# Optimization experiments

Measured on AMD Instinct MI355X. Metric: run time of the kernel, lower is better.

## Reference

```python
import jax, jax.numpy as jnp
import numpy as np
import math

V, L, D, S, F, H, B = 32000, 6, 1024, 2048, 4096, 16, 2
DK = D // H
EPS = 1e-5


def _pos_encoding(max_len, d_model):
    pos = np.arange(max_len)[:, None].astype(np.float32)
    freq = np.exp(np.arange(0, d_model, 2).astype(np.float32) * -(math.log(10000.0) / d_model))
    pe = np.zeros((max_len, d_model), dtype=np.float32)
    pe[:, 0::2] = np.sin(pos * freq)
    pe[:, 1::2] = np.cos(pos * freq)
    return jnp.asarray(pe)


def setup_inputs() -> dict:
    key = jax.random.key(0)
    ks = jax.random.split(key, 16)
    n = lambda k, shape: (jax.random.normal(k, shape, dtype=jnp.float32) * 0.02)
    return {
        "tokens": jax.random.randint(ks[0], (B, S), 0, V, dtype=jnp.int32),
        "emb": n(ks[1], (V, D)),
        "Wq": n(ks[2], (L, D, D)), "bq": jnp.zeros((L, D)),
        "Wk": n(ks[3], (L, D, D)), "bk": jnp.zeros((L, D)),
        "Wv": n(ks[4], (L, D, D)), "bv": jnp.zeros((L, D)),
        "Wo": n(ks[5], (L, D, D)), "bo": jnp.zeros((L, D)),
        "W1": n(ks[6], (L, D, F)), "b1": jnp.zeros((L, F)),
        "W2": n(ks[7], (L, F, D)), "b2": jnp.zeros((L, D)),
        "g1": jnp.ones((L, D)), "be1": jnp.zeros((L, D)),
        "g2": jnp.ones((L, D)), "be2": jnp.zeros((L, D)),
    }


def _layernorm(x, g, b):
    mu = jnp.mean(x, axis=-1, keepdims=True)
    var = jnp.var(x, axis=-1, keepdims=True)
    return (x - mu) * jax.lax.rsqrt(var + EPS) * g + b


def _encoder(tokens, emb, Wq, bq, Wk, bk, Wv, bv, Wo, bo, W1, b1, W2, b2, g1, be1, g2, be2):
    pe = _pos_encoding(S, D)
    x = emb[tokens] * jnp.float32(math.sqrt(D)) + pe  # [B,S,D]

    def layer(x, p):
        wq, bq_, wk, bk_, wv, bv_, wo, bo_, w1, b1_, w2, b2_, g1_, be1_, g2_, be2_ = p
        q = (x @ wq + bq_).reshape(B, S, H, DK)
        k = (x @ wk + bk_).reshape(B, S, H, DK)
        v = (x @ wv + bv_).reshape(B, S, H, DK)
        scores = jnp.einsum("bqhd,bkhd->bhqk", q, k) / jnp.float32(math.sqrt(DK))
        attn = jax.nn.softmax(scores, axis=-1)
        out = jnp.einsum("bhqk,bkhd->bqhd", attn, v).reshape(B, S, D)
        out = out @ wo + bo_
        x = _layernorm(x + out, g1_, be1_)
        ff = jax.nn.relu(x @ w1 + b1_) @ w2 + b2_
        x = _layernorm(x + ff, g2_, be2_)
        return x, None

    params = (Wq, bq, Wk, bk, Wv, bv, Wo, bo, W1, b1, W2, b2, g1, be1, g2, be2)
    x, _ = jax.lax.scan(layer, x, params)
    return x


def reference(tokens, emb, Wq, bq, Wk, bk, Wv, bv, Wo, bo, W1, b1, W2, b2, g1, be1, g2, be2):
    return _encoder(tokens, emb, Wq, bq, Wk, bk, Wv, bv, Wo, bo, W1, b1, W2, b2, g1, be1, g2, be2)
```

## Files before the change

kernel.cpp:

```cpp
#include <hip/hip_runtime.h>
#include <hip/hip_bf16.h>

#define DEV static __device__ __forceinline__

typedef __attribute__((ext_vector_type(8))) short bf16x8;
typedef __attribute__((ext_vector_type(4))) float f32x4;
typedef __attribute__((ext_vector_type(4))) unsigned short u16x4;
typedef __attribute__((ext_vector_type(4))) unsigned int u32x4;

constexpr int Lc = 6, Dc = 1024, Sc = 2048, Fc = 4096, Hc = 16, Bc = 2;
constexpr int Mc = Bc * Sc;
constexpr int QKVN = 3 * Dc;
constexpr float QSCALE = 0.18033688011112042f;

DEV float bf2f(unsigned short u) {
  unsigned int x = ((unsigned int)u) << 16; float f;
  __builtin_memcpy(&f, &x, 4); return f;
}
DEV unsigned short f2bf(float f) {
  unsigned int x; __builtin_memcpy(&x, &f, 4);
  x += 0x7fffu + ((x >> 16) & 1u);
  return (unsigned short)(x >> 16);
}
DEV unsigned int cvt_pk_bf16(float lo, float hi) {
  unsigned int r;
  asm("v_cvt_pk_bf16_f32 %0, %1, %2" : "=v"(r) : "v"(lo), "v"(hi));
  return r;
}

typedef __attribute__((address_space(1))) unsigned int* gas_t;
typedef __attribute__((address_space(3))) unsigned int* las_t;
DEV void gload16(const void* g, void* l) {
  __builtin_amdgcn_global_load_lds((gas_t)g, (las_t)l, 16, 0, 0);
}

__global__ __launch_bounds__(256) void transpose_f2b(
    const float* __restrict__ W, unsigned short* __restrict__ Wt,
    int Kd, int Nd, float scale)
{
  __shared__ float tile[32][33];
  const int n0 = blockIdx.x * 32, k0 = blockIdx.y * 32;
  const int tx = threadIdx.x & 31, ty = threadIdx.x >> 5;
#pragma unroll
  for (int i = 0; i < 4; ++i) {
    int k = ty + i * 8;
    tile[k][tx] = W[(size_t)(k0 + k) * Nd + n0 + tx];
  }
  __syncthreads();
#pragma unroll
  for (int i = 0; i < 4; ++i) {
    int n = ty + i * 8;
    Wt[(size_t)(n0 + n) * Kd + k0 + tx] = f2bf(tile[tx][n] * scale);
  }
}

DEV int vperm(int k) {
  return ((k >> 5) << 5) + (((k >> 2) & 3) << 3) + (((k >> 4) & 1) << 2) + (k & 3);
}
__global__ __launch_bounds__(256) void transpose_v(
    const unsigned short* __restrict__ QKV, unsigned short* __restrict__ Vt)
{
  __shared__ unsigned short tile[32][33];
  const int s0 = blockIdx.x * 32, c0 = blockIdx.y * 32, b = blockIdx.z;
  const int tx = threadIdx.x & 31, ty = threadIdx.x >> 5;
  const unsigned short* src = QKV + ((size_t)b * Sc) * QKVN + 2 * Dc;
#pragma unroll
  for (int i = 0; i < 4; ++i) {
    int s = ty + i * 8;
    tile[s][tx] = src[(size_t)(s0 + s) * QKVN + c0 + tx];
  }
  __syncthreads();
  unsigned short* dst = Vt + (size_t)b * Dc * Sc;
  const int s = s0 + tx;
  const int sp = (s & ~63) + vperm(s & 63);
#pragma unroll
  for (int i = 0; i < 4; ++i) {
    int c = ty + i * 8;
    dst[(size_t)(c0 + c) * Sc + sp] = tile[tx][c];
  }
}

__global__ __launch_bounds__(256) void pack_bias(
    const float* __restrict__ bq, const float* __restrict__ bk,
    const float* __restrict__ bv, float* __restrict__ out)
{
  int i = blockIdx.x * 256 + threadIdx.x;
  out[i] = (i < Dc) ? bq[i] * QSCALE : (i < 2 * Dc ? bk[i - Dc] : bv[i - 2 * Dc]);
}

__global__ __launch_bounds__(256) void embed_kernel(
    const int* __restrict__ tokens, const float* __restrict__ emb,
    float* __restrict__ xf, unsigned short* __restrict__ xb)
{
  const int bs = blockIdx.x;
  const int s = bs & (Sc - 1);
  const int tok = tokens[bs];
  const int d0 = threadIdx.x * 4;
  f32x4 e4 = *(const f32x4*)(emb + (size_t)tok * Dc + d0);
  f32x4 vf; u16x4 vb;
#pragma unroll
  for (int j = 0; j < 4; ++j) {
    int d = d0 + j;
    float e = e4[j] * 32.0f;
    float fr = expf((float)(d & ~1) * (-9.210340371976184f / 1024.0f));
    float arg = (float)s * fr;
    float pe = (d & 1) ? cosf(arg) : sinf(arg);
    float v = e + pe;
    vf[j] = v; vb[j] = f2bf(v);
  }
  *(f32x4*)(xf + (size_t)bs * Dc + d0) = vf;
  *(u16x4*)(xb + (size_t)bs * Dc + d0) = vb;
}

DEV void gemm_core(const unsigned short* A, const unsigned short* Bt,
                   unsigned short* As, unsigned short* Bs,
                   f32x4 (*acc)[4], int mTile, int nTile,
                   int Kstride, int k0, int k1, int t)
{
  const int lane = t & 63;
  const int w = t >> 6;
  const int wm = w >> 1, wn = w & 1;
  for (int kt = k0; kt < k1; kt += 64) {
    __syncthreads();
#pragma unroll
    for (int i = 0; i < 4; ++i) {
      int idx = i * 256 + t;
      int row = idx >> 3;
      int sl = (idx & 7) ^ (row & 7);
      gload16(A + (size_t)(mTile + row) * Kstride + kt + sl * 8, &As[idx * 8]);
      gload16(Bt + (size_t)(nTile + row) * Kstride + kt + sl * 8, &Bs[idx * 8]);
    }
    __syncthreads();
#pragma unroll
    for (int ks = 0; ks < 2; ++ks) {
      const int kb = ks * 64 + ((lane >> 4) << 4);
      bf16x8 a[4], b[4];
#pragma unroll
      for (int mi = 0; mi < 4; ++mi) {
        int r = wm * 64 + mi * 16 + (lane & 15);
        a[mi] = *(const bf16x8*)((const char*)As + r * 128 + (kb ^ ((r & 7) << 4)));
      }
#pragma unroll
      for (int ni = 0; ni < 4; ++ni) {
        int r = wn * 64 + ni * 16 + (lane & 15);
        b[ni] = *(const bf16x8*)((const char*)Bs + r * 128 + (kb ^ ((r & 7) << 4)));
      }
#pragma unroll
      for (int mi = 0; mi < 4; ++mi)
#pragma unroll
        for (int ni = 0; ni < 4; ++ni)
          acc[mi][ni] = __builtin_amdgcn_mfma_f32_16x16x32_bf16(
              a[mi], b[ni], acc[mi][ni], 0, 0, 0);
    }
  }
}

__global__ __launch_bounds__(256) void gemm128(
    const unsigned short* __restrict__ A, const unsigned short* __restrict__ Bt,
    const float* __restrict__ bias, unsigned short* __restrict__ outB,
    int gx, int Ndim, int Kdim, int relu)
{
  __shared__ alignas(16) unsigned short As[128 * 64];
  __shared__ alignas(16) unsigned short Bs[128 * 64];
  const int t = threadIdx.x;
  const int lane = t & 63;
  const int w = t >> 6;
  const int wm = w >> 1, wn = w & 1;
  const int nwg = gridDim.x, flat = blockIdx.x;
  const int swz = (flat & 7) * (nwg >> 3) + (flat >> 3);
  const int mTile = (swz / gx) * 128;
  const int nTile = (swz % gx) * 128;

  f32x4 acc[4][4] = {};
  gemm_core(A, Bt, As, Bs, acc, mTile, nTile, Kdim, 0, Kdim, t);

#pragma unroll
  for (int mi = 0; mi < 4; ++mi) {
#pragma unroll
    for (int ni = 0; ni < 4; ++ni) {
      const int c = nTile + wn * 64 + ni * 16 + (lane & 15);
      const float bvv = bias[c];
#pragma unroll
      for (int j = 0; j < 4; ++j) {
        const int r = mTile + wm * 64 + mi * 16 + ((lane >> 4) << 2) + j;
        float v = acc[mi][ni][j] + bvv;
        if (relu) v = fmaxf(v, 0.0f);
        outB[(size_t)r * Ndim + c] = f2bf(v);
      }
    }
  }
}

template<int SPLIT>
__global__ __launch_bounds__(256) void gemm_sk(
    const unsigned short* __restrict__ A, const unsigned short* __restrict__ Bt,
    float* __restrict__ part, int gx, int gy, int Ndim, int Ktot)
{
  __shared__ alignas(16) unsigned short As[128 * 64];
  __shared__ alignas(16) unsigned short Bs[128 * 64];
  const int t = threadIdx.x;
  const int lane = t & 63;
  const int w = t >> 6;
  const int wm = w >> 1, wn = w & 1;
  const int nwg = gridDim.x, flat = blockIdx.x;
  const int swz = (flat & 7) * (nwg >> 3) + (flat >> 3);
  const int nTile = (swz % gx) * 128;
  const int mTile = ((swz / gx) % gy) * 128;
  const int z = swz / (gx * gy);
  const int Kseg = Ktot / SPLIT;

  f32x4 acc[4][4] = {};
  gemm_core(A, Bt, As, Bs, acc, mTile, nTile, Ktot, z * Kseg, (z + 1) * Kseg, t);

  float* po = part + (size_t)z * Mc * Ndim;
#pragma unroll
  for (int mi = 0; mi < 4; ++mi)
#pragma unroll
    for (int ni = 0; ni < 4; ++ni) {
      const int c = nTile + wn * 64 + ni * 16 + (lane & 15);
#pragma unroll
      for (int j = 0; j < 4; ++j) {
        const int r = mTile + wm * 64 + mi * 16 + ((lane >> 4) << 2) + j;
        po[(size_t)r * Ndim + c] = acc[mi][ni][j];
      }
    }
}

__global__ __launch_bounds__(256) void attn64(
    const unsigned short* __restrict__ QKV, const unsigned short* __restrict__ Vt,
    unsigned short* __restrict__ O)
{
  __shared__ alignas(16) unsigned short Qs[64 * 64];
  __shared__ alignas(16) unsigned short Ks[64 * 64];
  __shared__ alignas(16) unsigned short Vs[64 * 64];

  const int t = threadIdx.x;
  const int lane = t & 63, w = t >> 6;
  const int g = lane >> 4, li = lane & 15;
  const int flat = blockIdx.x;
  const int idx = ((flat & 7) << 7) | (flat >> 3);
  const int qb = idx & 31, bh = idx >> 5;
  const int b = bh >> 4, h = bh & 15;

  const size_t qbase  = ((size_t)(b * Sc + qb * 64)) * QKVN + h * 64;
  const size_t kbase0 = ((size_t)b * Sc) * QKVN + Dc + h * 64;
  const size_t vbase0 = ((size_t)(b * Dc + h * 64)) * Sc;

  const unsigned short* kg[2];
  const unsigned short* vg[2];
  unsigned short* kl[2];
  unsigned short* vl[2];
#pragma unroll
  for (int i = 0; i < 2; ++i) {
    int idx2 = i * 256 + t, row = idx2 >> 3, sl = (idx2 & 7) ^ (row & 7);
    gload16(QKV + qbase + (size_t)row * QKVN + sl * 8, &Qs[idx2 * 8]);
    kg[i] = QKV + kbase0 + (size_t)row * QKVN + sl * 8;
    vg[i] = Vt + vbase0 + (size_t)row * Sc + sl * 8;
    kl[i] = &Ks[idx2 * 8];
    vl[i] = &Vs[idx2 * 8];
  }
  __syncthreads();
  bf16x8 qf[2];
  {
    const int rq = w * 16 + li;
#pragma unroll
    for (int ks = 0; ks < 2; ++ks) {
      const int kb = ks * 64 + (g << 4);
      qf[ks] = *(const bf16x8*)((const char*)Qs + rq * 128 + (kb ^ ((rq & 7) << 4)));
    }
  }
  bf16x8 ones;
#pragma unroll
  for (int e = 0; e < 8; ++e) ones[e] = (short)0x3F80;

  f32x4 acc_o[4] = {};
  f32x4 acc_l = {};

  for (int kc = 0; kc < Sc; kc += 64) {
    __syncthreads();
    gload16(kg[0], kl[0]); gload16(kg[1], kl[1]);
    gload16(vg[0], vl[0]); gload16(vg[1], vl[1]);
    kg[0] += 64 * QKVN; kg[1] += 64 * QKVN;
    vg[0] += 64;        vg[1] += 64;
    __syncthreads();

    f32x4 accs[4] = {};
#pragma unroll
    for (int ks = 0; ks < 2; ++ks) {
      const int kb = ks * 64 + (g << 4);
#pragma unroll
      for (int ni = 0; ni < 4; ++ni) {
        int rk = ni * 16 + li;
        bf16x8 ak = *(const bf16x8*)((const char*)Ks + rk * 128 + (kb ^ ((rk & 7) << 4)));
        accs[ni] = __builtin_amdgcn_mfma_f32_16x16x32_bf16(ak, qf[ks], accs[ni], 0, 0, 0);
      }
    }

    unsigned int pk[4][2];
#pragma unroll
    for (int ni = 0; ni < 4; ++ni) {
      float p0 = exp2f(accs[ni][0]);
      float p1 = exp2f(accs[ni][1]);
      float p2 = exp2f(accs[ni][2]);
      float p3 = exp2f(accs[ni][3]);
      pk[ni][0] = cvt_pk_bf16(p0, p1);
      pk[ni][1] = cvt_pk_bf16(p2, p3);
    }

#pragma unroll
    for (int ks = 0; ks < 2; ++ks) {
      u32x4 av = {pk[2 * ks][0], pk[2 * ks][1], pk[2 * ks + 1][0], pk[2 * ks + 1][1]};
      bf16x8 ap = __builtin_bit_cast(bf16x8, av);
      const int kb = ks * 64 + (g << 4);
      acc_l = __builtin_amdgcn_mfma_f32_16x16x32_bf16(ap, ones, acc_l, 0, 0, 0);
#pragma unroll
      for (int ni = 0; ni < 4; ++ni) {
        int rd = ni * 16 + li;
        bf16x8 bv = *(const bf16x8*)((const char*)Vs + rd * 128 + (kb ^ ((rd & 7) << 4)));
        acc_o[ni] = __builtin_amdgcn_mfma_f32_16x16x32_bf16(ap, bv, acc_o[ni], 0, 0, 0);
      }
    }
  }

  float denom[4];
#pragma unroll
  for (int j = 0; j < 4; ++j) denom[j] = 1.0f / acc_l[j];

  const size_t obase = ((size_t)(b * Sc + qb * 64)) * Dc + h * 64;
#pragma unroll
  for (int ni = 0; ni < 4; ++ni)
#pragma unroll
    for (int j = 0; j < 4; ++j) {
      int q = w * 16 + g * 4 + j;
      O[obase + (size_t)q * Dc + ni * 16 + li] = f2bf(acc_o[ni][j] * denom[j]);
    }
}

template<int SPLIT>
__global__ __launch_bounds__(256) void reduce_ln(
    const float* __restrict__ part, const float* __restrict__ bias,
    const float* __restrict__ res, const float* __restrict__ g,
    const float* __restrict__ be, float* __restrict__ xf_out,
    unsigned short* __restrict__ xb_out)
{
  const int row = blockIdx.x, t = threadIdx.x;
  const size_t off = (size_t)row * Dc + t * 4;
  f32x4 v = *(const f32x4*)(res + off);
  v += *(const f32x4*)(bias + t * 4);
#pragma unroll
  for (int s = 0; s < SPLIT; ++s)
    v += *(const f32x4*)(part + (size_t)s * Mc * Dc + off);

  float sm = v[0] + v[1] + v[2] + v[3];
  float q = v[0]*v[0] + v[1]*v[1] + v[2]*v[2] + v[3]*v[3];
#pragma unroll
  for (int o = 32; o; o >>= 1) {
    sm += __shfl_down(sm, o);
    q += __shfl_down(q, o);
  }
  __shared__ float rs_[4], rq_[4];
  const int lane = t & 63, w = t >> 6;
  if (lane == 0) { rs_[w] = sm; rq_[w] = q; }
  __syncthreads();
  sm = rs_[0] + rs_[1] + rs_[2] + rs_[3];
  q = rq_[0] + rq_[1] + rq_[2] + rq_[3];
  const float mu = sm * (1.0f / 1024.0f);
  const float var = q * (1.0f / 1024.0f) - mu * mu;
  const float rstd = rsqrtf(var + 1e-5f);
  f32x4 vg = *(const f32x4*)(g + t * 4);
  f32x4 vb = *(const f32x4*)(be + t * 4);
  f32x4 o; u16x4 ob;
#pragma unroll
  for (int j = 0; j < 4; ++j) {
    float val = (v[j] - mu) * rstd * vg[j] + vb[j];
    o[j] = val; ob[j] = f2bf(val);
  }
  *(f32x4*)(xf_out + off) = o;
  *(u16x4*)(xb_out + off) = ob;
}

extern "C" void kernel_launch(void* const* d_in, const int* in_sizes, int n_in,
                              void* d_out, int out_size, void* d_ws, size_t ws_size,
                              hipStream_t stream)
{
  (void)in_sizes; (void)n_in; (void)out_size; (void)ws_size;
  const int*   tokens = (const int*)d_in[0];
  const float* emb = (const float*)d_in[1];
  const float* Wq = (const float*)d_in[2];
  const float* bq = (const float*)d_in[3];
  const float* Wk = (const float*)d_in[4];
  const float* bk = (const float*)d_in[5];
  const float* Wv = (const float*)d_in[6];
  const float* bv = (const float*)d_in[7];
  const float* Wo = (const float*)d_in[8];
  const float* bo = (const float*)d_in[9];
  const float* W1 = (const float*)d_in[10];
  const float* b1 = (const float*)d_in[11];
  const float* W2 = (const float*)d_in[12];
  const float* b2 = (const float*)d_in[13];
  const float* g1 = (const float*)d_in[14];
  const float* be1 = (const float*)d_in[15];
  const float* g2 = (const float*)d_in[16];
  const float* be2 = (const float*)d_in[17];

  char* p = (char*)d_ws;
  auto take = [&](size_t bytes) { char* q = p; p += bytes; return q; };
  unsigned short* Wqkvt = (unsigned short*)take((size_t)3 * Dc * Dc * 2);
  unsigned short* Wot = (unsigned short*)take((size_t)Dc * Dc * 2);
  unsigned short* W1t = (unsigned short*)take((size_t)Dc * Fc * 2);
  unsigned short* W2t = (unsigned short*)take((size_t)Fc * Dc * 2);
  float*          bqkv = (float*)take((size_t)QKVN * 4);
  float*          xf  = (float*)take((size_t)Mc * Dc * 4);
  unsigned short* xb  = (unsigned short*)take((size_t)Mc * Dc * 2);
  unsigned short* QKVb = (unsigned short*)take((size_t)Mc * QKVN * 2);
  unsigned short* Vtb = (unsigned short*)take((size_t)Bc * Dc * Sc * 2);
  unsigned short* Ob  = (unsigned short*)take((size_t)Mc * Dc * 2);
  unsigned short* ff1 = (unsigned short*)take((size_t)Mc * Fc * 2);
  float* part = (float*)QKVb;

  dim3 blk(256);
  embed_kernel<<<dim3(Mc), blk, 0, stream>>>(tokens, emb, xf, xb);

  for (int l = 0; l < Lc; ++l) {
    const size_t owD = (size_t)l * Dc * Dc;
    const size_t owF = (size_t)l * Dc * Fc;
    const int ob = l * Dc;
    transpose_f2b<<<dim3(Dc / 32, Dc / 32), blk, 0, stream>>>(Wq + owD, Wqkvt, Dc, Dc, QSCALE);
    transpose_f2b<<<dim3(Dc / 32, Dc / 32), blk, 0, stream>>>(Wk + owD, Wqkvt + (size_t)Dc * Dc, Dc, Dc, 1.0f);
    transpose_f2b<<<dim3(Dc / 32, Dc / 32), blk, 0, stream>>>(Wv + owD, Wqkvt + (size_t)2 * Dc * Dc, Dc, Dc, 1.0f);
    transpose_f2b<<<dim3(Dc / 32, Dc / 32), blk, 0, stream>>>(Wo + owD, Wot, Dc, Dc, 1.0f);
    transpose_f2b<<<dim3(Fc / 32, Dc / 32), blk, 0, stream>>>(W1 + owF, W1t, Dc, Fc, 1.0f);
    transpose_f2b<<<dim3(Dc / 32, Fc / 32), blk, 0, stream>>>(W2 + owF, W2t, Fc, Dc, 1.0f);
    pack_bias<<<dim3(QKVN / 256), blk, 0, stream>>>(bq + ob, bk + ob, bv + ob, bqkv);

    gemm128<<<dim3((QKVN / 128) * (Mc / 128)), blk, 0, stream>>>(
        xb, Wqkvt, bqkv, QKVb, QKVN / 128, QKVN, Dc, 0);
    transpose_v<<<dim3(Sc / 32, Dc / 32, Bc), blk, 0, stream>>>(QKVb, Vtb);
    attn64<<<dim3(1024), blk, 0, stream>>>(QKVb, Vtb, Ob);

    gemm_sk<2><<<dim3((Dc / 128) * (Mc / 128) * 2), blk, 0, stream>>>(
        Ob, Wot, part, Dc / 128, Mc / 128, Dc, Dc);
    reduce_ln<2><<<dim3(Mc), blk, 0, stream>>>(
        part, bo + ob, xf, g1 + ob, be1 + ob, xf, xb);

    gemm128<<<dim3((Fc / 128) * (Mc / 128)), blk, 0, stream>>>(
        xb, W1t, b1 + l * Fc, ff1, Fc / 128, Fc, Dc, 1);

    gemm_sk<2><<<dim3((Dc / 128) * (Mc / 128) * 2), blk, 0, stream>>>(
        ff1, W2t, part, Dc / 128, Mc / 128, Dc, Fc);
    reduce_ln<2><<<dim3(Mc), blk, 0, stream>>>(
        part, b2 + ob, xf, g2 + ob, be2 + ob,
        (l == Lc - 1) ? (float*)d_out : xf, xb);
  }
}
```

Before: 1.628 ms.

## Enlarge attention query tile to 128 and double-buffer K/V loads

```diff
diff --git a/kernel.cpp b/kernel.cpp
--- a/kernel.cpp
+++ b/kernel.cpp
@@ -226,114 +226,138 @@
     }
 }
 
-__global__ __launch_bounds__(256) void attn64(
+__global__ __launch_bounds__(256) void attn128(
     const unsigned short* __restrict__ QKV, const unsigned short* __restrict__ Vt,
     unsigned short* __restrict__ O)
 {
-  __shared__ alignas(16) unsigned short Qs[64 * 64];
-  __shared__ alignas(16) unsigned short Ks[64 * 64];
-  __shared__ alignas(16) unsigned short Vs[64 * 64];
+  __shared__ alignas(16) unsigned short Qs[128 * 64];
+  __shared__ alignas(16) unsigned short Ks[2][64 * 64];
+  __shared__ alignas(16) unsigned short Vs[2][64 * 64];
 
   const int t = threadIdx.x;
   const int lane = t & 63, w = t >> 6;
   const int g = lane >> 4, li = lane & 15;
   const int flat = blockIdx.x;
-  const int idx = ((flat & 7) << 7) | (flat >> 3);
-  const int qb = idx & 31, bh = idx >> 5;
+  const int idx = ((flat & 7) << 6) | (flat >> 3);
+  const int qb = idx & 15, bh = idx >> 4;
   const int b = bh >> 4, h = bh & 15;
 
-  const size_t qbase  = ((size_t)(b * Sc + qb * 64)) * QKVN + h * 64;
+  const size_t qbase  = ((size_t)(b * Sc + qb * 128)) * QKVN + h * 64;
   const size_t kbase0 = ((size_t)b * Sc) * QKVN + Dc + h * 64;
   const size_t vbase0 = ((size_t)(b * Dc + h * 64)) * Sc;
 
+#pragma unroll
+  for (int i = 0; i < 4; ++i) {
+    int idx2 = i * 256 + t, row = idx2 >> 3, sl = (idx2 & 7) ^ (row & 7);
+    gload16(QKV + qbase + (size_t)row * QKVN + sl * 8, &Qs[idx2 * 8]);
+  }
   const unsigned short* kg[2];
   const unsigned short* vg[2];
-  unsigned short* kl[2];
-  unsigned short* vl[2];
+  int loff[2];
 #pragma unroll
   for (int i = 0; i < 2; ++i) {
     int idx2 = i * 256 + t, row = idx2 >> 3, sl = (idx2 & 7) ^ (row & 7);
-    gload16(QKV + qbase + (size_t)row * QKVN + sl * 8, &Qs[idx2 * 8]);
     kg[i] = QKV + kbase0 + (size_t)row * QKVN + sl * 8;
     vg[i] = Vt + vbase0 + (size_t)row * Sc + sl * 8;
-    kl[i] = &Ks[idx2 * 8];
-    vl[i] = &Vs[idx2 * 8];
-  }
+    loff[i] = idx2 * 8;
+  }
+  gload16(kg[0], &Ks[0][loff[0]]); gload16(kg[1], &Ks[0][loff[1]]);
+  gload16(vg[0], &Vs[0][loff[0]]); gload16(vg[1], &Vs[0][loff[1]]);
+  kg[0] += 64 * QKVN; kg[1] += 64 * QKVN;
+  vg[0] += 64;        vg[1] += 64;
   __syncthreads();
-  bf16x8 qf[2];
-  {
-    const int rq = w * 16 + li;
+
+  bf16x8 qf[2][2];
+#pragma unroll
+  for (int qi = 0; qi < 2; ++qi) {
+    const int rq = w * 32 + qi * 16 + li;
 #pragma unroll
     for (int ks = 0; ks < 2; ++ks) {
       const int kb = ks * 64 + (g << 4);
-      qf[ks] = *(const bf16x8*)((const char*)Qs + rq * 128 + (kb ^ ((rq & 7) << 4)));
+      qf[qi][ks] = *(const bf16x8*)((const char*)Qs + rq * 128 + (kb ^ ((rq & 7) << 4)));
     }
   }
   bf16x8 ones;
 #pragma unroll
   for (int e = 0; e < 8; ++e) ones[e] = (short)0x3F80;
 
-  f32x4 acc_o[4] = {};
-  f32x4 acc_l = {};
+  f32x4 acc_o[2][4] = {};
+  f32x4 acc_l[2] = {};
+  int cur = 0;
 
   for (int kc = 0; kc < Sc; kc += 64) {
-    __syncthreads();
-    gload16(kg[0], kl[0]); gload16(kg[1], kl[1]);
-    gload16(vg[0], vl[0]); gload16(vg[1], vl[1]);
-    kg[0] += 64 * QKVN; kg[1] += 64 * QKVN;
-    vg[0] += 64;        vg[1] += 64;
-    __syncthreads();
-
-    f32x4 accs[4] = {};
+    if (kc + 64 < Sc) {
+      const int nxt = cur ^ 1;
+      gload16(kg[0], &Ks[nxt][loff[0]]); gload16(kg[1], &Ks[nxt][loff[1]]);
+      gload16(vg[0], &Vs[nxt][loff[0]]); gload16(vg[1], &Vs[nxt][loff[1]]);
+      kg[0] += 64 * QKVN; kg[1] += 64 * QKVN;
+      vg[0] += 64;        vg[1] += 64;
+    }
+
+    f32x4 accs[2][4] = {};
 #pragma unroll
     for (int ks = 0; ks < 2; ++ks) {
       const int kb = ks * 64 + (g << 4);
 #pragma unroll
       for (int ni = 0; ni < 4; ++ni) {
         int rk = ni * 16 + li;
-        bf16x8 ak = *(const bf16x8*)((const char*)Ks + rk * 128 + (kb ^ ((rk & 7) << 4)));
-        accs[ni] = __builtin_amdgcn_mfma_f32_16x16x32_bf16(ak, qf[ks], accs[ni], 0, 0, 0);
-      }
-    }
-
-    unsigned int pk[4][2];
-#pragma unroll
-    for (int ni = 0; ni < 4; ++ni) {
-      float p0 = exp2f(accs[ni][0]);
-      float p1 = exp2f(accs[ni][1]);
-      float p2 = exp2f(accs[ni][2]);
-      float p3 = exp2f(accs[ni][3]);
-      pk[ni][0] = cvt_pk_bf16(p0, p1);
-      pk[ni][1] = cvt_pk_bf16(p2, p3);
-    }
+        bf16x8 ak = *(const bf16x8*)((const char*)Ks[cur] + rk * 128 + (kb ^ ((rk & 7) << 4)));
+        accs[0][ni] = __builtin_amdgcn_mfma_f32_16x16x32_bf16(ak, qf[0][ks], accs[0][ni], 0, 0, 0);
+        accs[1][ni] = __builtin_amdgcn_mfma_f32_16x16x32_bf16(ak, qf[1][ks], accs[1][ni], 0, 0, 0);
+      }
+    }
+
+    unsigned int pk[2][4][2];
+#pragma unroll
+    for (int qi = 0; qi < 2; ++qi)
+#pragma unroll
+      for (int ni = 0; ni < 4; ++ni) {
+        float p0 = exp2f(accs[qi][ni][0]);
+        float p1 = exp2f(accs[qi][ni][1]);
+        float p2 = exp2f(accs[qi][ni][2]);
+        float p3 = exp2f(accs[qi][ni][3]);
+        pk[qi][ni][0] = cvt_pk_bf16(p0, p1);
+        pk[qi][ni][1] = cvt_pk_bf16(p2, p3);
+      }
 
 #pragma unroll
     for (int ks = 0; ks < 2; ++ks) {
-      u32x4 av = {pk[2 * ks][0], pk[2 * ks][1], pk[2 * ks + 1][0], pk[2 * ks + 1][1]};
-      bf16x8 ap = __builtin_bit_cast(bf16x8, av);
+      bf16x8 ap[2];
+#pragma unroll
+      for (int qi = 0; qi < 2; ++qi) {
+        u32x4 av = {pk[qi][2 * ks][0], pk[qi][2 * ks][1],
+                    pk[qi][2 * ks + 1][0], pk[qi][2 * ks + 1][1]};
+        ap[qi] = __builtin_bit_cast(bf16x8, av);
+        acc_l[qi] = __builtin_amdgcn_mfma_f32_16x16x32_bf16(ap[qi], ones, acc_l[qi], 0, 0, 0);
+      }
       const int kb = ks * 64 + (g << 4);
-      acc_l = __builtin_amdgcn_mfma_f32_16x16x32_bf16(ap, ones, acc_l, 0, 0, 0);
 #pragma unroll
       for (int ni = 0; ni < 4; ++ni) {
         int rd = ni * 16 + li;
-        bf16x8 bv = *(const bf16x8*)((const char*)Vs + rd * 128 + (kb ^ ((rd & 7) << 4)));
-        acc_o[ni] = __builtin_amdgcn_mfma_f32_16x16x32_bf16(ap, bv, acc_o[ni], 0, 0, 0);
-      }
-    }
-  }
-
-  float denom[4];
-#pragma unroll
-  for (int j = 0; j < 4; ++j) denom[j] = 1.0f / acc_l[j];
-
-  const size_t obase = ((size_t)(b * Sc + qb * 64)) * Dc + h * 64;
-#pragma unroll
-  for (int ni = 0; ni < 4; ++ni)
-#pragma unroll
-    for (int j = 0; j < 4; ++j) {
-      int q = w * 16 + g * 4 + j;
-      O[obase + (size_t)q * Dc + ni * 16 + li] = f2bf(acc_o[ni][j] * denom[j]);
-    }
+        bf16x8 bv = *(const bf16x8*)((const char*)Vs[cur] + rd * 128 + (kb ^ ((rd & 7) << 4)));
+        acc_o[0][ni] = __builtin_amdgcn_mfma_f32_16x16x32_bf16(ap[0], bv, acc_o[0][ni], 0, 0, 0);
+        acc_o[1][ni] = __builtin_amdgcn_mfma_f32_16x16x32_bf16(ap[1], bv, acc_o[1][ni], 0, 0, 0);
+      }
+    }
+
+    __syncthreads();
+    cur ^= 1;
+  }
+
+  const size_t obase = ((size_t)(b * Sc + qb * 128)) * Dc + h * 64;
+#pragma unroll
+  for (int qi = 0; qi < 2; ++qi) {
+    float denom[4];
+#pragma unroll
+    for (int j = 0; j < 4; ++j) denom[j] = 1.0f / acc_l[qi][j];
+#pragma unroll
+    for (int ni = 0; ni < 4; ++ni)
+#pragma unroll
+      for (int j = 0; j < 4; ++j) {
+        int q = w * 32 + qi * 16 + g * 4 + j;
+        O[obase + (size_t)q * Dc + ni * 16 + li] = f2bf(acc_o[qi][ni][j] * denom[j]);
+      }
+  }
 }
 
 template<int SPLIT>
@@ -436,7 +460,7 @@
     gemm128<<<dim3((QKVN / 128) * (Mc / 128)), blk, 0, stream>>>(
         xb, Wqkvt, bqkv, QKVb, QKVN / 128, QKVN, Dc, 0);
     transpose_v<<<dim3(Sc / 32, Dc / 32, Bc), blk, 0, stream>>>(QKVb, Vtb);
-    attn64<<<dim3(1024), blk, 0, stream>>>(QKVb, Vtb, Ob);
+    attn128<<<dim3(512), blk, 0, stream>>>(QKVb, Vtb, Ob);
 
     gemm_sk<2><<<dim3((Dc / 128) * (Mc / 128) * 2), blk, 0, stream>>>(
         Ob, Wot, part, Dc / 128, Mc / 128, Dc, Dc);
```

Measured after the change: 1.602 ms. About the same (-1.6%).
